# Performance work log

Hardware: AMD Instinct MI355X
Metric: run time of the kernel (lower is better)

Reference implementation:

```python
import jax, jax.numpy as jnp
import numpy as np

N_NODES, N_EDGES = 100000, 1600000
D_IN, D_HID, D_OUT = 128, 128, 64


def setup_inputs() -> dict:
    key = jax.random.key(0)
    k = jax.random.split(key, 6)
    x = jax.random.normal(k[0], (N_NODES, D_IN), dtype=jnp.float32)
    edge_index = jax.random.randint(k[1], (2, N_EDGES), 0, N_NODES, dtype=jnp.int32)
    # GCNConv params: W stored as [in, out] for right-multiply, glorot-ish scale
    W1 = jax.random.normal(k[2], (D_IN, D_HID), dtype=jnp.float32) * (1.0 / np.sqrt(D_IN))
    b1 = jnp.zeros((D_HID,), dtype=jnp.float32)
    W2 = jax.random.normal(k[3], (D_HID, D_OUT), dtype=jnp.float32) * (1.0 / np.sqrt(D_HID))
    b2 = jnp.zeros((D_OUT,), dtype=jnp.float32)
    return {"x": x, "edge_index": edge_index, "W1": W1, "b1": b1, "W2": W2, "b2": b2}


def reference(x, edge_index, W1, b1, W2, b2):
    N = x.shape[0]
    loops = jnp.arange(N, dtype=edge_index.dtype)
    src = jnp.concatenate([edge_index[0], loops])  # [E+N]
    dst = jnp.concatenate([edge_index[1], loops])  # [E+N]
    # symmetric GCN normalization (deg over targets, incl. self loops)
    deg = jax.ops.segment_sum(jnp.ones_like(dst, dtype=x.dtype), dst, num_segments=N)
    dinv = jnp.where(deg > 0, jax.lax.rsqrt(deg), 0.0)
    norm = dinv[src] * dinv[dst]  # [E+N]

    def gcn(h, W, b):
        h = h @ W                         # [N, out]
        msg = h[src] * norm[:, None]      # gather + scale, [E+N, out]
        return jax.ops.segment_sum(msg, dst, num_segments=N) + b

    h = jax.nn.relu(gcn(x, W1, b1))  # Dropout is identity in eval
    return gcn(h, W2, b2)
```

## Files before the change

### kernel.cpp

```cpp
#include <hip/hip_runtime.h>


#define D_IN  128
#define D_HID 128
#define D_OUT 64
#define NBSHIFT 9

typedef short short8 __attribute__((ext_vector_type(8)));
typedef float floatx4 __attribute__((ext_vector_type(4)));

__device__ __forceinline__ unsigned short f2bf(float f) {
    unsigned int u = __float_as_uint(f);
    u += 0x7fffu + ((u >> 16) & 1u);
    return (unsigned short)(u >> 16);
}
__device__ __forceinline__ float bf2f(unsigned short h) {
    return __uint_as_float((unsigned int)h << 16);
}
__device__ __forceinline__ float bf_lo(unsigned int u) { return __uint_as_float(u << 16); }
__device__ __forceinline__ float bf_hi(unsigned int u) { return __uint_as_float(u & 0xffff0000u); }


__global__ __launch_bounds__(256) void k_zero_int(int* __restrict__ p, int n) {
    int i = blockIdx.x * 256 + threadIdx.x;
    if (i < n) p[i] = 0;
}

__global__ __launch_bounds__(256) void k_bhist(const int* __restrict__ dst,
                                               int* __restrict__ bcnt, int E, int NB) {
    __shared__ int h[256];
    const int t = threadIdx.x;
    h[t] = 0;
    __syncthreads();
    const int base = blockIdx.x * 8192;
#pragma unroll
    for (int k = 0; k < 32; ++k) {
        int e = base + k * 256 + t;
        if (e < E) atomicAdd(&h[dst[e] >> NBSHIFT], 1);
    }
    __syncthreads();
    if (t < NB && h[t]) atomicAdd(&bcnt[t], h[t]);
}

__global__ __launch_bounds__(256) void k_bscan(const int* __restrict__ bcnt,
                                               int* __restrict__ bbase,
                                               int* __restrict__ bcur, int NB, int E) {
    __shared__ int ls[256];
    const int t = threadIdx.x;
    int v = (t < NB) ? bcnt[t] : 0;
    ls[t] = v;
    __syncthreads();
    for (int off = 1; off < 256; off <<= 1) {
        int y = (t >= off) ? ls[t - off] : 0;
        __syncthreads();
        ls[t] += y;
        __syncthreads();
    }
    if (t < NB) {
        bbase[t] = ls[t] - v;
        bcur[t]  = ls[t] - v;
    }
    if (t == 0) bbase[NB] = E;
}

__global__ __launch_bounds__(256) void k_bin(const int* __restrict__ src,
                                             const int* __restrict__ dst,
                                             int2* __restrict__ ebuf,
                                             int* __restrict__ bcur, int E, int NB) {
    __shared__ int h[256];
    __shared__ int basep[256];
    const int t = threadIdx.x;
    h[t] = 0;
    __syncthreads();
    const int base = blockIdx.x * 4096;
    int s[16], d[16];
#pragma unroll
    for (int k = 0; k < 16; ++k) {
        int e = base + k * 256 + t;
        bool v = e < E;
        s[k] = v ? src[e] : 0;
        d[k] = v ? dst[e] : -1;
        if (v) atomicAdd(&h[d[k] >> NBSHIFT], 1);
    }
    __syncthreads();
    if (t < NB && h[t]) basep[t] = atomicAdd(&bcur[t], h[t]);
    __syncthreads();
    h[t] = 0;
    __syncthreads();
#pragma unroll
    for (int k = 0; k < 16; ++k) {
        if (d[k] >= 0) {
            int b = d[k] >> NBSHIFT;
            int r = atomicAdd(&h[b], 1);
            ebuf[basep[b] + r] = make_int2(s[k], d[k]);
        }
    }
}

__global__ __launch_bounds__(256) void k_bfill(const int2* __restrict__ ebuf,
                                               const int* __restrict__ bbase,
                                               int* __restrict__ csr,
                                               int* __restrict__ rowstart,
                                               float* __restrict__ dinv,
                                               int N, int NB, int E) {
    __shared__ int cnt[512];
    __shared__ int pref[512];
    __shared__ int tsum[256];
    const int t = threadIdx.x;
    const int b = blockIdx.x;
    const int nb0 = b << NBSHIFT;
    const int NN = min(512, N - nb0);
    const int e0 = bbase[b], e1 = bbase[b + 1];

    cnt[t] = 0;
    cnt[t + 256] = 0;
    __syncthreads();
    for (int e = e0 + t; e < e1; e += 256)
        atomicAdd(&cnt[ebuf[e].y - nb0], 1);
    __syncthreads();

    int a0 = cnt[2 * t], a1 = cnt[2 * t + 1];
    tsum[t] = a0 + a1;
    __syncthreads();
    for (int off = 1; off < 256; off <<= 1) {
        int y = (t >= off) ? tsum[t - off] : 0;
        __syncthreads();
        tsum[t] += y;
        __syncthreads();
    }
    int excl = tsum[t] - (a0 + a1);
    pref[2 * t] = excl;
    pref[2 * t + 1] = excl + a0;
    __syncthreads();

    for (int nl = t; nl < NN; nl += 256) {
        rowstart[nb0 + nl] = e0 + pref[nl];
        dinv[nb0 + nl] = rsqrtf((float)(cnt[nl] + 1));
    }
    if (b == NB - 1 && t == 0) rowstart[N] = E;
    __syncthreads();

    for (int e = e0 + t; e < e1; e += 256) {
        int2 ed = ebuf[e];
        int r = atomicAdd(&pref[ed.y - nb0], 1);
        csr[e0 + r] = ed.x;
    }
}

__global__ void k_zero_pad(unsigned short* __restrict__ h1b,
                           unsigned short* __restrict__ h2b, int N) {
    int t = threadIdx.x;
    if (t < 128) h1b[(size_t)N * 128 + t] = 0;
    if (t < 64)  h2b[(size_t)N * 64 + t] = 0;
}


template <int DOUT_>
__global__ __launch_bounds__(256) void k_wsplit(const float* __restrict__ W,
                                                unsigned short* __restrict__ Ws) {
    constexpr int NCT = DOUT_ / 16;
    constexpr int HALF = 4 * NCT * 64 * 8;
    int id = blockIdx.x * 256 + threadIdx.x;
    if (id >= HALF) return;
    int i = id & 7;
    int lane = (id >> 3) & 63;
    int ctkt = id >> 9;
    int ct = ctkt % NCT, kt = ctkt / NCT;
    int k = kt * 32 + ((lane >> 4) << 3) + i;
    int n = ct * 16 + (lane & 15);
    float v = W[(size_t)k * DOUT_ + n];
    unsigned short h = f2bf(v);
    Ws[id] = h;
    Ws[HALF + id] = f2bf(v - bf2f(h));
}


template <int DOUT_>
__global__ __launch_bounds__(256) void mfma_gemm(const float* __restrict__ X,
                                                 const unsigned short* __restrict__ Wsplit,
                                                 const float* __restrict__ dinv,
                                                 unsigned short* __restrict__ Hb,
                                                 int N) {
    constexpr int NCT = DOUT_ / 16;
    constexpr int HALF = 4 * NCT * 64 * 8;
    __shared__ unsigned short lds[2 * HALF];

    const int t = threadIdx.x;
    {
        const int4* s4 = (const int4*)Wsplit;
        int4* d4 = (int4*)lds;
        constexpr int NV = 2 * HALF / 8;
        for (int i = t; i < NV; i += 256) d4[i] = s4[i];
    }
    __syncthreads();

    const int wave = t >> 6, lane = t & 63;
    const int grow = blockIdx.x * 64 + wave * 16 + (lane & 15);
    const int rowc = min(grow, N - 1);
    const int kl = (lane >> 4) << 3;

    floatx4 acc[NCT];
#pragma unroll
    for (int c = 0; c < NCT; ++c) acc[c] = (floatx4)0.f;

#pragma unroll
    for (int kt = 0; kt < 4; ++kt) {
        const float* xp = X + (size_t)rowc * 128 + kt * 32 + kl;
        float4 a0 = *(const float4*)xp;
        float4 a1 = *(const float4*)(xp + 4);
        float xs[8] = {a0.x, a0.y, a0.z, a0.w, a1.x, a1.y, a1.z, a1.w};
        short8 ah, al;
#pragma unroll
        for (int i = 0; i < 8; ++i) {
            unsigned short h = f2bf(xs[i]);
            ah[i] = (short)h;
            al[i] = (short)f2bf(xs[i] - bf2f(h));
        }
#pragma unroll
        for (int c = 0; c < NCT; ++c) {
            const int off = ((kt * NCT + c) * 64 + lane) * 8;
            short8 bh = *(const short8*)&lds[off];
            short8 bl = *(const short8*)&lds[HALF + off];
            acc[c] = __builtin_amdgcn_mfma_f32_16x16x32_bf16(ah, bh, acc[c], 0, 0, 0);
            acc[c] = __builtin_amdgcn_mfma_f32_16x16x32_bf16(al, bh, acc[c], 0, 0, 0);
            acc[c] = __builtin_amdgcn_mfma_f32_16x16x32_bf16(ah, bl, acc[c], 0, 0, 0);
        }
    }

    const int orow = blockIdx.x * 64 + wave * 16 + ((lane >> 4) << 2);
#pragma unroll
    for (int r = 0; r < 4; ++r) {
        int gr = orow + r;
        if (gr < N) {
            float dn = dinv[gr];
#pragma unroll
            for (int c = 0; c < NCT; ++c)
                Hb[(size_t)gr * DOUT_ + c * 16 + (lane & 15)] = f2bf(acc[c][r] * dn);
        }
    }
}


template <int DOUT_>
__global__ __launch_bounds__(256) void mfma_gemm_b(const unsigned short* __restrict__ Xb,
                                                   const unsigned short* __restrict__ Wsplit,
                                                   const float* __restrict__ dinv,
                                                   unsigned short* __restrict__ Hb,
                                                   int N) {
    constexpr int NCT = DOUT_ / 16;
    constexpr int HALF = 4 * NCT * 64 * 8;
    __shared__ unsigned short lds[2 * HALF];

    const int t = threadIdx.x;
    {
        const int4* s4 = (const int4*)Wsplit;
        int4* d4 = (int4*)lds;
        constexpr int NV = 2 * HALF / 8;
        for (int i = t; i < NV; i += 256) d4[i] = s4[i];
    }
    __syncthreads();

    const int wave = t >> 6, lane = t & 63;
    const int grow = blockIdx.x * 64 + wave * 16 + (lane & 15);
    const int rowc = min(grow, N - 1);
    const int kl = (lane >> 4) << 3;

    floatx4 acc[NCT];
#pragma unroll
    for (int c = 0; c < NCT; ++c) acc[c] = (floatx4)0.f;

#pragma unroll
    for (int kt = 0; kt < 4; ++kt) {
        short8 ah = *(const short8*)(Xb + (size_t)rowc * 128 + kt * 32 + kl);
#pragma unroll
        for (int c = 0; c < NCT; ++c) {
            const int off = ((kt * NCT + c) * 64 + lane) * 8;
            short8 bh = *(const short8*)&lds[off];
            short8 bl = *(const short8*)&lds[HALF + off];
            acc[c] = __builtin_amdgcn_mfma_f32_16x16x32_bf16(ah, bh, acc[c], 0, 0, 0);
            acc[c] = __builtin_amdgcn_mfma_f32_16x16x32_bf16(ah, bl, acc[c], 0, 0, 0);
        }
    }

    const int orow = blockIdx.x * 64 + wave * 16 + ((lane >> 4) << 2);
#pragma unroll
    for (int r = 0; r < 4; ++r) {
        int gr = orow + r;
        if (gr < N) {
            float dn = dinv[gr];
#pragma unroll
            for (int c = 0; c < NCT; ++c)
                Hb[(size_t)gr * DOUT_ + c * 16 + (lane & 15)] = f2bf(acc[c][r] * dn);
        }
    }
}


__global__ __launch_bounds__(256) void agg1_kernel(const uint4* __restrict__ H4,
                                                   const int* __restrict__ rowstart,
                                                   const int* __restrict__ csr_src,
                                                   const float* __restrict__ dinv,
                                                   const float* __restrict__ bias,
                                                   unsigned short* __restrict__ outb,
                                                   int N, int NBK) {
    const int xcd = blockIdx.x & 7;
    const int ch  = xcd >> 2;
    const int nb  = (blockIdx.x >> 3) * 4 + (xcd & 3);
    if (nb >= NBK) return;
    const int t = threadIdx.x;
    const int wave = t >> 6, lane = t & 63;
    const int g = lane >> 3, gl = lane & 7;
    const int n = nb * 32 + wave * 8 + g;
    const bool live = n < N;
    const int e0 = live ? rowstart[n] : 0;
    const int deg = live ? rowstart[n + 1] - e0 : 0;
    int m = deg;
    m = max(m, __shfl_xor(m, 8));
    m = max(m, __shfl_xor(m, 16));
    m = max(m, __shfl_xor(m, 32));

    const int cb = ch * 8;
    float acc[8] = {0.f, 0.f, 0.f, 0.f, 0.f, 0.f, 0.f, 0.f};
    for (int eb = 0; eb < m; eb += 8) {
        int s_l = (eb + gl < deg) ? csr_src[e0 + eb + gl] : N;
        int sj[8]; uint4 u[8];
#pragma unroll
        for (int q = 0; q < 8; ++q) sj[q] = __shfl(s_l, (g << 3) | q);
#pragma unroll
        for (int q = 0; q < 8; ++q) u[q] = H4[(size_t)sj[q] * 16 + cb + gl];
#pragma unroll
        for (int q = 0; q < 8; ++q) {
            acc[0] += bf_lo(u[q].x); acc[1] += bf_hi(u[q].x);
            acc[2] += bf_lo(u[q].y); acc[3] += bf_hi(u[q].y);
            acc[4] += bf_lo(u[q].z); acc[5] += bf_hi(u[q].z);
            acc[6] += bf_lo(u[q].w); acc[7] += bf_hi(u[q].w);
        }
    }
    uint4 us = H4[(size_t)(live ? n : N) * 16 + cb + gl];
    acc[0] += bf_lo(us.x); acc[1] += bf_hi(us.x);
    acc[2] += bf_lo(us.y); acc[3] += bf_hi(us.y);
    acc[4] += bf_lo(us.z); acc[5] += bf_hi(us.z);
    acc[6] += bf_lo(us.w); acc[7] += bf_hi(us.w);

    if (live) {
        const float dn = dinv[n];
        const float* bp = bias + ch * 64 + gl * 8;
        unsigned short o[8];
#pragma unroll
        for (int j = 0; j < 8; ++j)
            o[j] = f2bf(fmaxf(fmaf(acc[j], dn, bp[j]), 0.f));
        *reinterpret_cast<int4*>(&outb[(size_t)n * 128 + ch * 64 + gl * 8]) =
            *reinterpret_cast<const int4*>(o);
    }
}

__global__ __launch_bounds__(256) void agg2_kernel(const uint4* __restrict__ H4,
                                                   const int* __restrict__ rowstart,
                                                   const int* __restrict__ csr_src,
                                                   const float* __restrict__ dinv,
                                                   const float* __restrict__ bias,
                                                   float* __restrict__ out, int N) {
    const int t = threadIdx.x;
    const int wave = t >> 6, lane = t & 63;
    const int g = lane >> 3, gl = lane & 7;
    const int n = blockIdx.x * 32 + wave * 8 + g;
    const bool live = n < N;
    const int e0 = live ? rowstart[n] : 0;
    const int e1 = live ? rowstart[n + 1] : 0;
    const int deg = e1 - e0;
    int m = deg;
    m = max(m, __shfl_xor(m, 8));
    m = max(m, __shfl_xor(m, 16));
    m = max(m, __shfl_xor(m, 32));

    float acc[8] = {0.f, 0.f, 0.f, 0.f, 0.f, 0.f, 0.f, 0.f};
    for (int eb = 0; eb < m; eb += 8) {
        int s_l = (eb + gl < deg) ? csr_src[e0 + eb + gl] : N;
        int sj[8]; uint4 u[8];
#pragma unroll
        for (int q = 0; q < 8; ++q) sj[q] = __shfl(s_l, (g << 3) | q);
#pragma unroll
        for (int q = 0; q < 8; ++q) u[q] = H4[(size_t)sj[q] * 8 + gl];
#pragma unroll
        for (int q = 0; q < 8; ++q) {
            acc[0] += bf_lo(u[q].x); acc[1] += bf_hi(u[q].x);
            acc[2] += bf_lo(u[q].y); acc[3] += bf_hi(u[q].y);
            acc[4] += bf_lo(u[q].z); acc[5] += bf_hi(u[q].z);
            acc[6] += bf_lo(u[q].w); acc[7] += bf_hi(u[q].w);
        }
    }
    uint4 us = H4[(size_t)(live ? n : N) * 8 + gl];
    acc[0] += bf_lo(us.x); acc[1] += bf_hi(us.x);
    acc[2] += bf_lo(us.y); acc[3] += bf_hi(us.y);
    acc[4] += bf_lo(us.z); acc[5] += bf_hi(us.z);
    acc[6] += bf_lo(us.w); acc[7] += bf_hi(us.w);

    if (live) {
        const float dn = dinv[n];
        float4 o0, o1;
        o0.x = fmaf(acc[0], dn, bias[gl * 8 + 0]);
        o0.y = fmaf(acc[1], dn, bias[gl * 8 + 1]);
        o0.z = fmaf(acc[2], dn, bias[gl * 8 + 2]);
        o0.w = fmaf(acc[3], dn, bias[gl * 8 + 3]);
        o1.x = fmaf(acc[4], dn, bias[gl * 8 + 4]);
        o1.y = fmaf(acc[5], dn, bias[gl * 8 + 5]);
        o1.z = fmaf(acc[6], dn, bias[gl * 8 + 6]);
        o1.w = fmaf(acc[7], dn, bias[gl * 8 + 7]);
        float* op = out + (size_t)n * 64 + gl * 8;
        *reinterpret_cast<float4*>(op) = o0;
        *reinterpret_cast<float4*>(op + 4) = o1;
    }
}


extern "C" void kernel_launch(void* const* d_in, const int* in_sizes, int n_in,
                              void* d_out, int out_size, void* d_ws, size_t ws_size,
                              hipStream_t stream) {
    const float* x  = (const float*)d_in[0];
    const int*   ei = (const int*)d_in[1];
    const float* W1 = (const float*)d_in[2];
    const float* b1 = (const float*)d_in[3];
    const float* W2 = (const float*)d_in[4];
    const float* b2 = (const float*)d_in[5];
    float* out = (float*)d_out;

    const int N = in_sizes[0] / D_IN;
    const int E = in_sizes[1] / 2;
    const int* src = ei;
    const int* dst = ei + E;
    const int NB = (N + 511) >> NBSHIFT;

    char* w = (char*)d_ws;
    auto alloc = [&](size_t bytes) {
        char* p = w;
        w += (bytes + 255) & ~(size_t)255;
        return p;
    };
    int*   rowstart  = (int*)alloc((size_t)(N + 1) * 4);
    float* dinv      = (float*)alloc((size_t)N * 4);
    int*   csr       = (int*)alloc((size_t)E * 4);
    unsigned short* h1b = (unsigned short*)alloc((size_t)(N + 1) * D_HID * 2);
    unsigned short* h2b = (unsigned short*)alloc((size_t)(N + 1) * D_OUT * 2);
    unsigned short* hgb = (unsigned short*)alloc((size_t)N * D_HID * 2);
    int*   bcnt      = (int*)alloc((size_t)NB * 4);
    int*   bbase     = (int*)alloc((size_t)(NB + 1) * 4);
    int*   bcur      = (int*)alloc((size_t)NB * 4);
    unsigned short* w1s = (unsigned short*)alloc(2 * 4 * (D_HID / 16) * 64 * 8 * 2);
    unsigned short* w2s = (unsigned short*)alloc(2 * 4 * (D_OUT / 16) * 64 * 8 * 2);
    int2*  ebuf      = (int2*)hgb;

    k_zero_int<<<1, 256, 0, stream>>>(bcnt, NB);
    k_bhist<<<(E + 8191) / 8192, 256, 0, stream>>>(dst, bcnt, E, NB);
    k_bscan<<<1, 256, 0, stream>>>(bcnt, bbase, bcur, NB, E);
    k_bin<<<(E + 4095) / 4096, 256, 0, stream>>>(src, dst, ebuf, bcur, E, NB);
    k_bfill<<<NB, 256, 0, stream>>>(ebuf, bbase, csr, rowstart, dinv, N, NB, E);
    k_zero_pad<<<1, 128, 0, stream>>>(h1b, h2b, N);
    k_wsplit<D_HID><<<(4 * (D_HID / 16) * 64 * 8 + 255) / 256, 256, 0, stream>>>(W1, w1s);
    k_wsplit<D_OUT><<<(4 * (D_OUT / 16) * 64 * 8 + 255) / 256, 256, 0, stream>>>(W2, w2s);

    mfma_gemm<D_HID><<<(N + 63) / 64, 256, 0, stream>>>(x, w1s, dinv, h1b, N);

    const int NBK = (N + 31) / 32;
    agg1_kernel<<<((NBK + 3) / 4) * 8, 256, 0, stream>>>((const uint4*)h1b, rowstart, csr,
                                                         dinv, b1, hgb, N, NBK);
    mfma_gemm_b<D_OUT><<<(N + 63) / 64, 256, 0, stream>>>(hgb, w2s, dinv, h2b, N);
    agg2_kernel<<<(N + 31) / 32, 256, 0, stream>>>((const uint4*)h2b, rowstart, csr,
                                                   dinv, b2, out, N);
}
```

Measured before the change: 198.0 us.

## Store hidden features column-chunked and partition aggregation by 16-wide feature slices

```diff
diff --git a/kernel.cpp b/kernel.cpp
--- a/kernel.cpp
+++ b/kernel.cpp
@@ -150,8 +150,8 @@
 __global__ void k_zero_pad(unsigned short* __restrict__ h1b,
                            unsigned short* __restrict__ h2b, int N) {
     int t = threadIdx.x;
-    if (t < 128) h1b[(size_t)N * 128 + t] = 0;
-    if (t < 64)  h2b[(size_t)N * 64 + t] = 0;
+    if (t < 128) h1b[((size_t)(t >> 4) * (N + 1) + N) * 16 + (t & 15)] = 0;
+    if (t < 64)  h2b[((size_t)(t >> 4) * (N + 1) + N) * 16 + (t & 15)] = 0;
 }
 
 
@@ -235,7 +235,7 @@
             float dn = dinv[gr];
 #pragma unroll
             for (int c = 0; c < NCT; ++c)
-                Hb[(size_t)gr * DOUT_ + c * 16 + (lane & 15)] = f2bf(acc[c][r] * dn);
+                Hb[((size_t)c * (N + 1) + gr) * 16 + (lane & 15)] = f2bf(acc[c][r] * dn);
         }
     }
 }
@@ -271,7 +271,8 @@
 
 #pragma unroll
     for (int kt = 0; kt < 4; ++kt) {
-        short8 ah = *(const short8*)(Xb + (size_t)rowc * 128 + kt * 32 + kl);
+        const int k0 = kt * 32 + kl;
+        short8 ah = *(const short8*)&Xb[((size_t)(k0 >> 4) * N + rowc) * 16 + (k0 & 15)];
 #pragma unroll
         for (int c = 0; c < NCT; ++c) {
             const int off = ((kt * NCT + c) * 64 + lane) * 8;
@@ -290,7 +291,7 @@
             float dn = dinv[gr];
 #pragma unroll
             for (int c = 0; c < NCT; ++c)
-                Hb[(size_t)gr * DOUT_ + c * 16 + (lane & 15)] = f2bf(acc[c][r] * dn);
+                Hb[((size_t)c * (N + 1) + gr) * 16 + (lane & 15)] = f2bf(acc[c][r] * dn);
         }
     }
 }
@@ -301,33 +302,36 @@
                                                    const int* __restrict__ csr_src,
                                                    const float* __restrict__ dinv,
                                                    const float* __restrict__ bias,
-                                                   unsigned short* __restrict__ outb,
-                                                   int N, int NBK) {
-    const int xcd = blockIdx.x & 7;
-    const int ch  = xcd >> 2;
-    const int nb  = (blockIdx.x >> 3) * 4 + (xcd & 3);
-    if (nb >= NBK) return;
+                                                   unsigned short* __restrict__ outc,
+                                                   int N) {
+    const int p = blockIdx.x & 7;
+    const int chunk = blockIdx.x >> 3;
     const int t = threadIdx.x;
     const int wave = t >> 6, lane = t & 63;
-    const int g = lane >> 3, gl = lane & 7;
-    const int n = nb * 32 + wave * 8 + g;
-    const bool live = n < N;
-    const int e0 = live ? rowstart[n] : 0;
-    const int deg = live ? rowstart[n + 1] - e0 : 0;
-    int m = deg;
-    m = max(m, __shfl_xor(m, 8));
-    m = max(m, __shfl_xor(m, 16));
-    m = max(m, __shfl_xor(m, 32));
-
-    const int cb = ch * 8;
+    const int g = lane >> 1, gl = lane & 1;
+    const int n = chunk * 128 + wave * 32 + g;
+    if (n >= N) return;
+    const uint4* __restrict__ Hp = H4 + (size_t)p * (N + 1) * 2;
+    const int e0 = rowstart[n];
+    const int deg = rowstart[n + 1] - e0;
+
     float acc[8] = {0.f, 0.f, 0.f, 0.f, 0.f, 0.f, 0.f, 0.f};
-    for (int eb = 0; eb < m; eb += 8) {
-        int s_l = (eb + gl < deg) ? csr_src[e0 + eb + gl] : N;
-        int sj[8]; uint4 u[8];
-#pragma unroll
-        for (int q = 0; q < 8; ++q) sj[q] = __shfl(s_l, (g << 3) | q);
-#pragma unroll
-        for (int q = 0; q < 8; ++q) u[q] = H4[(size_t)sj[q] * 16 + cb + gl];
+    for (int eb = 0; eb < deg; eb += 8) {
+        int s[4];
+#pragma unroll
+        for (int k = 0; k < 4; ++k) {
+            int idx = eb + 2 * k + gl;
+            s[k] = (idx < deg) ? __builtin_nontemporal_load(csr_src + e0 + idx) : N;
+        }
+        int sj[8];
+#pragma unroll
+        for (int k = 0; k < 4; ++k) {
+            sj[2 * k]     = __shfl(s[k], (g << 1));
+            sj[2 * k + 1] = __shfl(s[k], (g << 1) | 1);
+        }
+        uint4 u[8];
+#pragma unroll
+        for (int q = 0; q < 8; ++q) u[q] = Hp[(size_t)sj[q] * 2 + gl];
 #pragma unroll
         for (int q = 0; q < 8; ++q) {
             acc[0] += bf_lo(u[q].x); acc[1] += bf_hi(u[q].x);
@@ -336,22 +340,20 @@
             acc[6] += bf_lo(u[q].w); acc[7] += bf_hi(u[q].w);
         }
     }
-    uint4 us = H4[(size_t)(live ? n : N) * 16 + cb + gl];
+    uint4 us = Hp[(size_t)n * 2 + gl];
     acc[0] += bf_lo(us.x); acc[1] += bf_hi(us.x);
     acc[2] += bf_lo(us.y); acc[3] += bf_hi(us.y);
     acc[4] += bf_lo(us.z); acc[5] += bf_hi(us.z);
     acc[6] += bf_lo(us.w); acc[7] += bf_hi(us.w);
 
-    if (live) {
-        const float dn = dinv[n];
-        const float* bp = bias + ch * 64 + gl * 8;
-        unsigned short o[8];
-#pragma unroll
-        for (int j = 0; j < 8; ++j)
-            o[j] = f2bf(fmaxf(fmaf(acc[j], dn, bp[j]), 0.f));
-        *reinterpret_cast<int4*>(&outb[(size_t)n * 128 + ch * 64 + gl * 8]) =
-            *reinterpret_cast<const int4*>(o);
-    }
+    const float dn = dinv[n];
+    const float* bp = bias + p * 16 + gl * 8;
+    unsigned short o[8];
+#pragma unroll
+    for (int j = 0; j < 8; ++j)
+        o[j] = f2bf(fmaxf(fmaf(acc[j], dn, bp[j]), 0.f));
+    *reinterpret_cast<uint4*>(&outc[((size_t)p * N + n) * 16 + gl * 8]) =
+        *reinterpret_cast<const uint4*>(o);
 }
 
 __global__ __launch_bounds__(256) void agg2_kernel(const uint4* __restrict__ H4,
@@ -359,28 +361,38 @@
                                                    const int* __restrict__ csr_src,
                                                    const float* __restrict__ dinv,
                                                    const float* __restrict__ bias,
-                                                   float* __restrict__ out, int N) {
+                                                   float* __restrict__ out,
+                                                   int N, int NCH) {
+    const int slot = blockIdx.x & 7;
+    const int p = slot & 3;
+    const int chunk = (blockIdx.x >> 3) * 2 + (slot >> 2);
+    if (chunk >= NCH) return;
     const int t = threadIdx.x;
     const int wave = t >> 6, lane = t & 63;
-    const int g = lane >> 3, gl = lane & 7;
-    const int n = blockIdx.x * 32 + wave * 8 + g;
-    const bool live = n < N;
-    const int e0 = live ? rowstart[n] : 0;
-    const int e1 = live ? rowstart[n + 1] : 0;
-    const int deg = e1 - e0;
-    int m = deg;
-    m = max(m, __shfl_xor(m, 8));
-    m = max(m, __shfl_xor(m, 16));
-    m = max(m, __shfl_xor(m, 32));
+    const int g = lane >> 1, gl = lane & 1;
+    const int n = chunk * 128 + wave * 32 + g;
+    if (n >= N) return;
+    const uint4* __restrict__ Hp = H4 + (size_t)p * (N + 1) * 2;
+    const int e0 = rowstart[n];
+    const int deg = rowstart[n + 1] - e0;
 
     float acc[8] = {0.f, 0.f, 0.f, 0.f, 0.f, 0.f, 0.f, 0.f};
-    for (int eb = 0; eb < m; eb += 8) {
-        int s_l = (eb + gl < deg) ? csr_src[e0 + eb + gl] : N;
-        int sj[8]; uint4 u[8];
-#pragma unroll
-        for (int q = 0; q < 8; ++q) sj[q] = __shfl(s_l, (g << 3) | q);
-#pragma unroll
-        for (int q = 0; q < 8; ++q) u[q] = H4[(size_t)sj[q] * 8 + gl];
+    for (int eb = 0; eb < deg; eb += 8) {
+        int s[4];
+#pragma unroll
+        for (int k = 0; k < 4; ++k) {
+            int idx = eb + 2 * k + gl;
+            s[k] = (idx < deg) ? __builtin_nontemporal_load(csr_src + e0 + idx) : N;
+        }
+        int sj[8];
+#pragma unroll
+        for (int k = 0; k < 4; ++k) {
+            sj[2 * k]     = __shfl(s[k], (g << 1));
+            sj[2 * k + 1] = __shfl(s[k], (g << 1) | 1);
+        }
+        uint4 u[8];
+#pragma unroll
+        for (int q = 0; q < 8; ++q) u[q] = Hp[(size_t)sj[q] * 2 + gl];
 #pragma unroll
         for (int q = 0; q < 8; ++q) {
             acc[0] += bf_lo(u[q].x); acc[1] += bf_hi(u[q].x);
@@ -389,27 +401,26 @@
             acc[6] += bf_lo(u[q].w); acc[7] += bf_hi(u[q].w);
         }
     }
-    uint4 us = H4[(size_t)(live ? n : N) * 8 + gl];
+    uint4 us = Hp[(size_t)n * 2 + gl];
     acc[0] += bf_lo(us.x); acc[1] += bf_hi(us.x);
     acc[2] += bf_lo(us.y); acc[3] += bf_hi(us.y);
     acc[4] += bf_lo(us.z); acc[5] += bf_hi(us.z);
     acc[6] += bf_lo(us.w); acc[7] += bf_hi(us.w);
 
-    if (live) {
-        const float dn = dinv[n];
-        float4 o0, o1;
-        o0.x = fmaf(acc[0], dn, bias[gl * 8 + 0]);
-        o0.y = fmaf(acc[1], dn, bias[gl * 8 + 1]);
-        o0.z = fmaf(acc[2], dn, bias[gl * 8 + 2]);
-        o0.w = fmaf(acc[3], dn, bias[gl * 8 + 3]);
-        o1.x = fmaf(acc[4], dn, bias[gl * 8 + 4]);
-        o1.y = fmaf(acc[5], dn, bias[gl * 8 + 5]);
-        o1.z = fmaf(acc[6], dn, bias[gl * 8 + 6]);
-        o1.w = fmaf(acc[7], dn, bias[gl * 8 + 7]);
-        float* op = out + (size_t)n * 64 + gl * 8;
-        *reinterpret_cast<float4*>(op) = o0;
-        *reinterpret_cast<float4*>(op + 4) = o1;
-    }
+    const float dn = dinv[n];
+    const float* bp = bias + p * 16 + gl * 8;
+    float4 o0, o1;
+    o0.x = fmaf(acc[0], dn, bp[0]);
+    o0.y = fmaf(acc[1], dn, bp[1]);
+    o0.z = fmaf(acc[2], dn, bp[2]);
+    o0.w = fmaf(acc[3], dn, bp[3]);
+    o1.x = fmaf(acc[4], dn, bp[4]);
+    o1.y = fmaf(acc[5], dn, bp[5]);
+    o1.z = fmaf(acc[6], dn, bp[6]);
+    o1.w = fmaf(acc[7], dn, bp[7]);
+    float* op = out + (size_t)n * 64 + p * 16 + gl * 8;
+    *reinterpret_cast<float4*>(op) = o0;
+    *reinterpret_cast<float4*>(op + 4) = o1;
 }
 
 
@@ -458,12 +469,12 @@
     k_wsplit<D_HID><<<(4 * (D_HID / 16) * 64 * 8 + 255) / 256, 256, 0, stream>>>(W1, w1s);
     k_wsplit<D_OUT><<<(4 * (D_OUT / 16) * 64 * 8 + 255) / 256, 256, 0, stream>>>(W2, w2s);
 
+    const int NCH = (N + 127) / 128;
+
     mfma_gemm<D_HID><<<(N + 63) / 64, 256, 0, stream>>>(x, w1s, dinv, h1b, N);
-
-    const int NBK = (N + 31) / 32;
-    agg1_kernel<<<((NBK + 3) / 4) * 8, 256, 0, stream>>>((const uint4*)h1b, rowstart, csr,
-                                                         dinv, b1, hgb, N, NBK);
+    agg1_kernel<<<NCH * 8, 256, 0, stream>>>((const uint4*)h1b, rowstart, csr,
+                                             dinv, b1, hgb, N);
     mfma_gemm_b<D_OUT><<<(N + 63) / 64, 256, 0, stream>>>(hgb, w2s, dinv, h2b, N);
-    agg2_kernel<<<(N + 31) / 32, 256, 0, stream>>>((const uint4*)h2b, rowstart, csr,
-                                                   dinv, b2, out, N);
-}
+    agg2_kernel<<<((NCH + 1) / 2) * 8, 256, 0, stream>>>((const uint4*)h2b, rowstart, csr,
+                                                         dinv, b2, out, N, NCH);
+}
```

Measured after the change: 308.2 us. 1.56x slower.

## Pack binned edges into one int and sort CSR neighbors by source octant

Applied to the files above, without the earlier changes.

```diff
diff --git a/kernel.cpp b/kernel.cpp
--- a/kernel.cpp
+++ b/kernel.cpp
@@ -8,6 +8,7 @@
 
 typedef short short8 __attribute__((ext_vector_type(8)));
 typedef float floatx4 __attribute__((ext_vector_type(4)));
+typedef float floatx2 __attribute__((ext_vector_type(2)));
 
 __device__ __forceinline__ unsigned short f2bf(float f) {
     unsigned int u = __float_as_uint(f);
@@ -65,7 +66,7 @@
 
 __global__ __launch_bounds__(256) void k_bin(const int* __restrict__ src,
                                              const int* __restrict__ dst,
-                                             int2* __restrict__ ebuf,
+                                             int* __restrict__ ebuf,
                                              int* __restrict__ bcur, int E, int NB) {
     __shared__ int h[256];
     __shared__ int basep[256];
@@ -92,19 +93,19 @@
         if (d[k] >= 0) {
             int b = d[k] >> NBSHIFT;
             int r = atomicAdd(&h[b], 1);
-            ebuf[basep[b] + r] = make_int2(s[k], d[k]);
-        }
-    }
-}
-
-__global__ __launch_bounds__(256) void k_bfill(const int2* __restrict__ ebuf,
+            ebuf[basep[b] + r] = (s[k] << 9) | (d[k] & 511);
+        }
+    }
+}
+
+__global__ __launch_bounds__(256) void k_bfill(const int* __restrict__ ebuf,
                                                const int* __restrict__ bbase,
                                                int* __restrict__ csr,
                                                int* __restrict__ rowstart,
                                                float* __restrict__ dinv,
-                                               int N, int NB, int E) {
-    __shared__ int cnt[512];
-    __shared__ int pref[512];
+                                               int N, int NB, int E, int qshift) {
+    __shared__ int cnt2[512][8];
+    __shared__ int nbase[512];
     __shared__ int tsum[256];
     const int t = threadIdx.x;
     const int b = blockIdx.x;
@@ -112,15 +113,23 @@
     const int NN = min(512, N - nb0);
     const int e0 = bbase[b], e1 = bbase[b + 1];
 
-    cnt[t] = 0;
-    cnt[t + 256] = 0;
-    __syncthreads();
-    for (int e = e0 + t; e < e1; e += 256)
-        atomicAdd(&cnt[ebuf[e].y - nb0], 1);
-    __syncthreads();
-
-    int a0 = cnt[2 * t], a1 = cnt[2 * t + 1];
-    tsum[t] = a0 + a1;
+    for (int i = t; i < 512 * 8; i += 256) ((int*)cnt2)[i] = 0;
+    __syncthreads();
+    for (int e = e0 + t; e < e1; e += 256) {
+        int v = ebuf[e];
+        int nl = v & 511;
+        int o = ((unsigned)v >> 9) >> qshift;
+        atomicAdd(&cnt2[nl][o], 1);
+    }
+    __syncthreads();
+
+    int deg0 = 0, deg1 = 0;
+#pragma unroll
+    for (int o = 0; o < 8; ++o) {
+        deg0 += cnt2[2 * t][o];
+        deg1 += cnt2[2 * t + 1][o];
+    }
+    tsum[t] = deg0 + deg1;
     __syncthreads();
     for (int off = 1; off < 256; off <<= 1) {
         int y = (t >= off) ? tsum[t - off] : 0;
@@ -128,22 +137,37 @@
         tsum[t] += y;
         __syncthreads();
     }
-    int excl = tsum[t] - (a0 + a1);
-    pref[2 * t] = excl;
-    pref[2 * t + 1] = excl + a0;
-    __syncthreads();
-
+    int excl = tsum[t] - (deg0 + deg1);
+    nbase[2 * t] = excl;
+    nbase[2 * t + 1] = excl + deg0;
+    __syncthreads();
+
+#pragma unroll
+    for (int k = 0; k < 2; ++k) {
+        int nl = 2 * t + k;
+        int run = nbase[nl];
+#pragma unroll
+        for (int o = 0; o < 8; ++o) {
+            int c = cnt2[nl][o];
+            cnt2[nl][o] = run;
+            run += c;
+        }
+    }
     for (int nl = t; nl < NN; nl += 256) {
-        rowstart[nb0 + nl] = e0 + pref[nl];
-        dinv[nb0 + nl] = rsqrtf((float)(cnt[nl] + 1));
+        int deg = ((nl < 511 ? nbase[nl + 1] : e1 - e0)) - nbase[nl];
+        rowstart[nb0 + nl] = e0 + nbase[nl];
+        dinv[nb0 + nl] = rsqrtf((float)(deg + 1));
     }
     if (b == NB - 1 && t == 0) rowstart[N] = E;
     __syncthreads();
 
     for (int e = e0 + t; e < e1; e += 256) {
-        int2 ed = ebuf[e];
-        int r = atomicAdd(&pref[ed.y - nb0], 1);
-        csr[e0 + r] = ed.x;
+        int v = ebuf[e];
+        int nl = v & 511;
+        int srcv = (unsigned)v >> 9;
+        int o = srcv >> qshift;
+        int r = atomicAdd(&cnt2[nl][o], 1);
+        csr[e0 + r] = srcv;
     }
 }
 
@@ -322,7 +346,9 @@
     const int cb = ch * 8;
     float acc[8] = {0.f, 0.f, 0.f, 0.f, 0.f, 0.f, 0.f, 0.f};
     for (int eb = 0; eb < m; eb += 8) {
-        int s_l = (eb + gl < deg) ? csr_src[e0 + eb + gl] : N;
+        int s_l = (eb + gl < deg)
+                      ? __builtin_nontemporal_load(csr_src + e0 + eb + gl)
+                      : N;
         int sj[8]; uint4 u[8];
 #pragma unroll
         for (int q = 0; q < 8; ++q) sj[q] = __shfl(s_l, (g << 3) | q);
@@ -366,8 +392,7 @@
     const int n = blockIdx.x * 32 + wave * 8 + g;
     const bool live = n < N;
     const int e0 = live ? rowstart[n] : 0;
-    const int e1 = live ? rowstart[n + 1] : 0;
-    const int deg = e1 - e0;
+    const int deg = live ? rowstart[n + 1] - e0 : 0;
     int m = deg;
     m = max(m, __shfl_xor(m, 8));
     m = max(m, __shfl_xor(m, 16));
@@ -375,7 +400,9 @@
 
     float acc[8] = {0.f, 0.f, 0.f, 0.f, 0.f, 0.f, 0.f, 0.f};
     for (int eb = 0; eb < m; eb += 8) {
-        int s_l = (eb + gl < deg) ? csr_src[e0 + eb + gl] : N;
+        int s_l = (eb + gl < deg)
+                      ? __builtin_nontemporal_load(csr_src + e0 + eb + gl)
+                      : N;
         int sj[8]; uint4 u[8];
 #pragma unroll
         for (int q = 0; q < 8; ++q) sj[q] = __shfl(s_l, (g << 3) | q);
@@ -397,18 +424,19 @@
 
     if (live) {
         const float dn = dinv[n];
-        float4 o0, o1;
-        o0.x = fmaf(acc[0], dn, bias[gl * 8 + 0]);
-        o0.y = fmaf(acc[1], dn, bias[gl * 8 + 1]);
-        o0.z = fmaf(acc[2], dn, bias[gl * 8 + 2]);
-        o0.w = fmaf(acc[3], dn, bias[gl * 8 + 3]);
-        o1.x = fmaf(acc[4], dn, bias[gl * 8 + 4]);
-        o1.y = fmaf(acc[5], dn, bias[gl * 8 + 5]);
-        o1.z = fmaf(acc[6], dn, bias[gl * 8 + 6]);
-        o1.w = fmaf(acc[7], dn, bias[gl * 8 + 7]);
+        const float* bp = bias + gl * 8;
+        floatx4 o0, o1;
+        o0.x = fmaf(acc[0], dn, bp[0]);
+        o0.y = fmaf(acc[1], dn, bp[1]);
+        o0.z = fmaf(acc[2], dn, bp[2]);
+        o0.w = fmaf(acc[3], dn, bp[3]);
+        o1.x = fmaf(acc[4], dn, bp[4]);
+        o1.y = fmaf(acc[5], dn, bp[5]);
+        o1.z = fmaf(acc[6], dn, bp[6]);
+        o1.w = fmaf(acc[7], dn, bp[7]);
         float* op = out + (size_t)n * 64 + gl * 8;
-        *reinterpret_cast<float4*>(op) = o0;
-        *reinterpret_cast<float4*>(op + 4) = o1;
+        __builtin_nontemporal_store(o0, reinterpret_cast<floatx4*>(op));
+        __builtin_nontemporal_store(o1, reinterpret_cast<floatx4*>(op + 4));
     }
 }
 
@@ -429,6 +457,8 @@
     const int* src = ei;
     const int* dst = ei + E;
     const int NB = (N + 511) >> NBSHIFT;
+    int qshift = 0;
+    while (((N - 1) >> qshift) >= 8) ++qshift;
 
     char* w = (char*)d_ws;
     auto alloc = [&](size_t bytes) {
@@ -447,13 +477,13 @@
     int*   bcur      = (int*)alloc((size_t)NB * 4);
     unsigned short* w1s = (unsigned short*)alloc(2 * 4 * (D_HID / 16) * 64 * 8 * 2);
     unsigned short* w2s = (unsigned short*)alloc(2 * 4 * (D_OUT / 16) * 64 * 8 * 2);
-    int2*  ebuf      = (int2*)hgb;
+    int*   ebuf      = (int*)hgb;
 
     k_zero_int<<<1, 256, 0, stream>>>(bcnt, NB);
     k_bhist<<<(E + 8191) / 8192, 256, 0, stream>>>(dst, bcnt, E, NB);
     k_bscan<<<1, 256, 0, stream>>>(bcnt, bbase, bcur, NB, E);
     k_bin<<<(E + 4095) / 4096, 256, 0, stream>>>(src, dst, ebuf, bcur, E, NB);
-    k_bfill<<<NB, 256, 0, stream>>>(ebuf, bbase, csr, rowstart, dinv, N, NB, E);
+    k_bfill<<<NB, 256, 0, stream>>>(ebuf, bbase, csr, rowstart, dinv, N, NB, E, qshift);
     k_zero_pad<<<1, 128, 0, stream>>>(h1b, h2b, N);
     k_wsplit<D_HID><<<(4 * (D_HID / 16) * 64 * 8 + 255) / 256, 256, 0, stream>>>(W1, w1s);
     k_wsplit<D_OUT><<<(4 * (D_OUT / 16) * 64 * 8 + 255) / 256, 256, 0, stream>>>(W2, w2s);
```

Result: slower. 204.5 us (+3.3%).

## Replace global bucket histogram/scan with fixed-size segments and packed edge/node info

Applied to the files above, without the earlier changes.

```diff
diff --git a/kernel.cpp b/kernel.cpp
--- a/kernel.cpp
+++ b/kernel.cpp
@@ -5,6 +5,7 @@
 #define D_HID 128
 #define D_OUT 64
 #define NBSHIFT 9
+#define SEG 10240
 
 typedef short short8 __attribute__((ext_vector_type(8)));
 typedef float floatx4 __attribute__((ext_vector_type(4)));
@@ -21,150 +22,13 @@
 __device__ __forceinline__ float bf_hi(unsigned int u) { return __uint_as_float(u & 0xffff0000u); }
 
 
-__global__ __launch_bounds__(256) void k_zero_int(int* __restrict__ p, int n) {
-    int i = blockIdx.x * 256 + threadIdx.x;
-    if (i < n) p[i] = 0;
-}
-
-__global__ __launch_bounds__(256) void k_bhist(const int* __restrict__ dst,
-                                               int* __restrict__ bcnt, int E, int NB) {
-    __shared__ int h[256];
-    const int t = threadIdx.x;
-    h[t] = 0;
-    __syncthreads();
-    const int base = blockIdx.x * 8192;
-#pragma unroll
-    for (int k = 0; k < 32; ++k) {
-        int e = base + k * 256 + t;
-        if (e < E) atomicAdd(&h[dst[e] >> NBSHIFT], 1);
-    }
-    __syncthreads();
-    if (t < NB && h[t]) atomicAdd(&bcnt[t], h[t]);
-}
-
-__global__ __launch_bounds__(256) void k_bscan(const int* __restrict__ bcnt,
-                                               int* __restrict__ bbase,
-                                               int* __restrict__ bcur, int NB, int E) {
-    __shared__ int ls[256];
-    const int t = threadIdx.x;
-    int v = (t < NB) ? bcnt[t] : 0;
-    ls[t] = v;
-    __syncthreads();
-    for (int off = 1; off < 256; off <<= 1) {
-        int y = (t >= off) ? ls[t - off] : 0;
-        __syncthreads();
-        ls[t] += y;
-        __syncthreads();
-    }
-    if (t < NB) {
-        bbase[t] = ls[t] - v;
-        bcur[t]  = ls[t] - v;
-    }
-    if (t == 0) bbase[NB] = E;
-}
-
-__global__ __launch_bounds__(256) void k_bin(const int* __restrict__ src,
-                                             const int* __restrict__ dst,
-                                             int2* __restrict__ ebuf,
-                                             int* __restrict__ bcur, int E, int NB) {
-    __shared__ int h[256];
-    __shared__ int basep[256];
-    const int t = threadIdx.x;
-    h[t] = 0;
-    __syncthreads();
-    const int base = blockIdx.x * 4096;
-    int s[16], d[16];
-#pragma unroll
-    for (int k = 0; k < 16; ++k) {
-        int e = base + k * 256 + t;
-        bool v = e < E;
-        s[k] = v ? src[e] : 0;
-        d[k] = v ? dst[e] : -1;
-        if (v) atomicAdd(&h[d[k] >> NBSHIFT], 1);
-    }
-    __syncthreads();
-    if (t < NB && h[t]) basep[t] = atomicAdd(&bcur[t], h[t]);
-    __syncthreads();
-    h[t] = 0;
-    __syncthreads();
-#pragma unroll
-    for (int k = 0; k < 16; ++k) {
-        if (d[k] >= 0) {
-            int b = d[k] >> NBSHIFT;
-            int r = atomicAdd(&h[b], 1);
-            ebuf[basep[b] + r] = make_int2(s[k], d[k]);
-        }
-    }
-}
-
-__global__ __launch_bounds__(256) void k_bfill(const int2* __restrict__ ebuf,
-                                               const int* __restrict__ bbase,
-                                               int* __restrict__ csr,
-                                               int* __restrict__ rowstart,
-                                               float* __restrict__ dinv,
-                                               int N, int NB, int E) {
-    __shared__ int cnt[512];
-    __shared__ int pref[512];
-    __shared__ int tsum[256];
-    const int t = threadIdx.x;
-    const int b = blockIdx.x;
-    const int nb0 = b << NBSHIFT;
-    const int NN = min(512, N - nb0);
-    const int e0 = bbase[b], e1 = bbase[b + 1];
-
-    cnt[t] = 0;
-    cnt[t + 256] = 0;
-    __syncthreads();
-    for (int e = e0 + t; e < e1; e += 256)
-        atomicAdd(&cnt[ebuf[e].y - nb0], 1);
-    __syncthreads();
-
-    int a0 = cnt[2 * t], a1 = cnt[2 * t + 1];
-    tsum[t] = a0 + a1;
-    __syncthreads();
-    for (int off = 1; off < 256; off <<= 1) {
-        int y = (t >= off) ? tsum[t - off] : 0;
-        __syncthreads();
-        tsum[t] += y;
-        __syncthreads();
-    }
-    int excl = tsum[t] - (a0 + a1);
-    pref[2 * t] = excl;
-    pref[2 * t + 1] = excl + a0;
-    __syncthreads();
-
-    for (int nl = t; nl < NN; nl += 256) {
-        rowstart[nb0 + nl] = e0 + pref[nl];
-        dinv[nb0 + nl] = rsqrtf((float)(cnt[nl] + 1));
-    }
-    if (b == NB - 1 && t == 0) rowstart[N] = E;
-    __syncthreads();
-
-    for (int e = e0 + t; e < e1; e += 256) {
-        int2 ed = ebuf[e];
-        int r = atomicAdd(&pref[ed.y - nb0], 1);
-        csr[e0 + r] = ed.x;
-    }
-}
-
-__global__ void k_zero_pad(unsigned short* __restrict__ h1b,
-                           unsigned short* __restrict__ h2b, int N) {
-    int t = threadIdx.x;
-    if (t < 128) h1b[(size_t)N * 128 + t] = 0;
-    if (t < 64)  h2b[(size_t)N * 64 + t] = 0;
-}
-
-
-template <int DOUT_>
-__global__ __launch_bounds__(256) void k_wsplit(const float* __restrict__ W,
-                                                unsigned short* __restrict__ Ws) {
-    constexpr int NCT = DOUT_ / 16;
-    constexpr int HALF = 4 * NCT * 64 * 8;
-    int id = blockIdx.x * 256 + threadIdx.x;
-    if (id >= HALF) return;
+__device__ __forceinline__ void wsplit_one(const float* __restrict__ W,
+                                           unsigned short* __restrict__ Ws,
+                                           int id, int DOUT_, int HALF) {
     int i = id & 7;
     int lane = (id >> 3) & 63;
     int ctkt = id >> 9;
+    int NCT = DOUT_ / 16;
     int ct = ctkt % NCT, kt = ctkt / NCT;
     int k = kt * 32 + ((lane >> 4) << 3) + i;
     int n = ct * 16 + (lane & 15);
@@ -172,6 +36,107 @@
     unsigned short h = f2bf(v);
     Ws[id] = h;
     Ws[HALF + id] = f2bf(v - bf2f(h));
+}
+
+__global__ __launch_bounds__(256) void k_prep(const float* __restrict__ W1,
+                                              const float* __restrict__ W2,
+                                              unsigned short* __restrict__ w1s,
+                                              unsigned short* __restrict__ w2s,
+                                              unsigned short* __restrict__ h1b,
+                                              unsigned short* __restrict__ h2b,
+                                              int* __restrict__ bcur, int N) {
+    int id = blockIdx.x * 256 + threadIdx.x;
+    if (id < 16384) wsplit_one(W1, w1s, id, D_HID, 16384);
+    if (id < 8192)  wsplit_one(W2, w2s, id, D_OUT, 8192);
+    if (id < 128)   h1b[(size_t)N * 128 + id] = 0;
+    if (id < 64)    h2b[(size_t)N * 64 + id] = 0;
+    if (id < 256)   bcur[id] = 0;
+}
+
+
+__global__ __launch_bounds__(256) void k_bin(const int* __restrict__ src,
+                                             const int* __restrict__ dst,
+                                             int* __restrict__ ebuf,
+                                             int* __restrict__ bcur, int E, int NB) {
+    __shared__ int h[256];
+    __shared__ int basep[256];
+    const int t = threadIdx.x;
+    h[t] = 0;
+    __syncthreads();
+    const int base = blockIdx.x * 4096;
+    int s[16], d[16];
+#pragma unroll
+    for (int k = 0; k < 16; ++k) {
+        int e = base + k * 256 + t;
+        bool v = e < E;
+        s[k] = v ? src[e] : 0;
+        d[k] = v ? dst[e] : -1;
+        if (v) atomicAdd(&h[d[k] >> NBSHIFT], 1);
+    }
+    __syncthreads();
+    if (t < NB && h[t]) basep[t] = atomicAdd(&bcur[t], h[t]);
+    __syncthreads();
+    h[t] = 0;
+    __syncthreads();
+#pragma unroll
+    for (int k = 0; k < 16; ++k) {
+        if (d[k] >= 0) {
+            int b = d[k] >> NBSHIFT;
+            int r = atomicAdd(&h[b], 1);
+            ebuf[(size_t)b * SEG + basep[b] + r] = (s[k] << 9) | (d[k] & 511);
+        }
+    }
+}
+
+__global__ __launch_bounds__(256) void k_bfill(const int* __restrict__ ebuf,
+                                               const int* __restrict__ bcur,
+                                               int* __restrict__ csr,
+                                               int* __restrict__ nodeinfo,
+                                               float* __restrict__ dinv,
+                                               int N) {
+    __shared__ int cnt[512];
+    __shared__ int pref[512];
+    __shared__ int tsum[256];
+    const int t = threadIdx.x;
+    const int b = blockIdx.x;
+    const int nb0 = b << NBSHIFT;
+    const int NN = min(512, N - nb0);
+    const int ec = bcur[b];
+    const int* __restrict__ eb = ebuf + (size_t)b * SEG;
+
+    cnt[t] = 0;
+    cnt[t + 256] = 0;
+    __syncthreads();
+    for (int e = t; e < ec; e += 256) atomicAdd(&cnt[eb[e] & 511], 1);
+    __syncthreads();
+
+    int a0 = cnt[2 * t], a1 = cnt[2 * t + 1];
+    tsum[t] = a0 + a1;
+    __syncthreads();
+    for (int off = 1; off < 256; off <<= 1) {
+        int y = (t >= off) ? tsum[t - off] : 0;
+        __syncthreads();
+        tsum[t] += y;
+        __syncthreads();
+    }
+    int excl = tsum[t] - (a0 + a1);
+    pref[2 * t] = excl;
+    pref[2 * t + 1] = excl + a0;
+    __syncthreads();
+
+    const int segbase = b * SEG;
+    for (int nl = t; nl < NN; nl += 256) {
+        int deg = cnt[nl];
+        nodeinfo[nb0 + nl] = ((segbase + pref[nl]) << 10) | deg;
+        dinv[nb0 + nl] = rsqrtf((float)(deg + 1));
+    }
+    __syncthreads();
+
+    for (int e = t; e < ec; e += 256) {
+        int v = eb[e];
+        int r = atomicAdd(&pref[v & 511], 1);
+        csr[segbase + r] = (unsigned)v >> 9;
+    }
 }
 
 
@@ -297,7 +262,7 @@
 
 
 __global__ __launch_bounds__(256) void agg1_kernel(const uint4* __restrict__ H4,
-                                                   const int* __restrict__ rowstart,
+                                                   const int* __restrict__ nodeinfo,
                                                    const int* __restrict__ csr_src,
                                                    const float* __restrict__ dinv,
                                                    const float* __restrict__ bias,
@@ -312,8 +277,9 @@
     const int g = lane >> 3, gl = lane & 7;
     const int n = nb * 32 + wave * 8 + g;
     const bool live = n < N;
-    const int e0 = live ? rowstart[n] : 0;
-    const int deg = live ? rowstart[n + 1] - e0 : 0;
+    const int v = live ? nodeinfo[n] : 0;
+    const int e0 = (unsigned)v >> 10;
+    const int deg = v & 1023;
     int m = deg;
     m = max(m, __shfl_xor(m, 8));
     m = max(m, __shfl_xor(m, 16));
@@ -322,7 +288,9 @@
     const int cb = ch * 8;
     float acc[8] = {0.f, 0.f, 0.f, 0.f, 0.f, 0.f, 0.f, 0.f};
     for (int eb = 0; eb < m; eb += 8) {
-        int s_l = (eb + gl < deg) ? csr_src[e0 + eb + gl] : N;
+        int s_l = (eb + gl < deg)
+                      ? __builtin_nontemporal_load(csr_src + e0 + eb + gl)
+                      : N;
         int sj[8]; uint4 u[8];
 #pragma unroll
         for (int q = 0; q < 8; ++q) sj[q] = __shfl(s_l, (g << 3) | q);
@@ -354,61 +322,61 @@
     }
 }
 
-__global__ __launch_bounds__(256) void agg2_kernel(const uint4* __restrict__ H4,
-                                                   const int* __restrict__ rowstart,
+__global__ __launch_bounds__(256) void agg2_kernel(const uint2* __restrict__ H2,
+                                                   const int* __restrict__ nodeinfo,
                                                    const int* __restrict__ csr_src,
                                                    const float* __restrict__ dinv,
                                                    const float* __restrict__ bias,
-                                                   float* __restrict__ out, int N) {
+                                                   float* __restrict__ out,
+                                                   int N, int NBK) {
+    const int xcd = blockIdx.x & 7;
+    const int ch  = xcd >> 2;
+    const int nb  = (blockIdx.x >> 3) * 4 + (xcd & 3);
+    if (nb >= NBK) return;
     const int t = threadIdx.x;
     const int wave = t >> 6, lane = t & 63;
     const int g = lane >> 3, gl = lane & 7;
-    const int n = blockIdx.x * 32 + wave * 8 + g;
+    const int n = nb * 32 + wave * 8 + g;
     const bool live = n < N;
-    const int e0 = live ? rowstart[n] : 0;
-    const int e1 = live ? rowstart[n + 1] : 0;
-    const int deg = e1 - e0;
+    const int v = live ? nodeinfo[n] : 0;
+    const int e0 = (unsigned)v >> 10;
+    const int deg = v & 1023;
     int m = deg;
     m = max(m, __shfl_xor(m, 8));
     m = max(m, __shfl_xor(m, 16));
     m = max(m, __shfl_xor(m, 32));
 
-    float acc[8] = {0.f, 0.f, 0.f, 0.f, 0.f, 0.f, 0.f, 0.f};
+    const int cb = ch * 8;
+    float acc[4] = {0.f, 0.f, 0.f, 0.f};
     for (int eb = 0; eb < m; eb += 8) {
-        int s_l = (eb + gl < deg) ? csr_src[e0 + eb + gl] : N;
-        int sj[8]; uint4 u[8];
+        int s_l = (eb + gl < deg)
+                      ? __builtin_nontemporal_load(csr_src + e0 + eb + gl)
+                      : N;
+        int sj[8]; uint2 u[8];
 #pragma unroll
         for (int q = 0; q < 8; ++q) sj[q] = __shfl(s_l, (g << 3) | q);
 #pragma unroll
-        for (int q = 0; q < 8; ++q) u[q] = H4[(size_t)sj[q] * 8 + gl];
+        for (int q = 0; q < 8; ++q) u[q] = H2[(size_t)sj[q] * 16 + cb + gl];
 #pragma unroll
         for (int q = 0; q < 8; ++q) {
             acc[0] += bf_lo(u[q].x); acc[1] += bf_hi(u[q].x);
             acc[2] += bf_lo(u[q].y); acc[3] += bf_hi(u[q].y);
-            acc[4] += bf_lo(u[q].z); acc[5] += bf_hi(u[q].z);
-            acc[6] += bf_lo(u[q].w); acc[7] += bf_hi(u[q].w);
-        }
-    }
-    uint4 us = H4[(size_t)(live ? n : N) * 8 + gl];
+        }
+    }
+    uint2 us = H2[(size_t)(live ? n : N) * 16 + cb + gl];
     acc[0] += bf_lo(us.x); acc[1] += bf_hi(us.x);
     acc[2] += bf_lo(us.y); acc[3] += bf_hi(us.y);
-    acc[4] += bf_lo(us.z); acc[5] += bf_hi(us.z);
-    acc[6] += bf_lo(us.w); acc[7] += bf_hi(us.w);
 
     if (live) {
         const float dn = dinv[n];
-        float4 o0, o1;
-        o0.x = fmaf(acc[0], dn, bias[gl * 8 + 0]);
-        o0.y = fmaf(acc[1], dn, bias[gl * 8 + 1]);
-        o0.z = fmaf(acc[2], dn, bias[gl * 8 + 2]);
-        o0.w = fmaf(acc[3], dn, bias[gl * 8 + 3]);
-        o1.x = fmaf(acc[4], dn, bias[gl * 8 + 4]);
-        o1.y = fmaf(acc[5], dn, bias[gl * 8 + 5]);
-        o1.z = fmaf(acc[6], dn, bias[gl * 8 + 6]);
-        o1.w = fmaf(acc[7], dn, bias[gl * 8 + 7]);
-        float* op = out + (size_t)n * 64 + gl * 8;
-        *reinterpret_cast<float4*>(op) = o0;
-        *reinterpret_cast<float4*>(op + 4) = o1;
+        const int c0 = ch * 32 + gl * 4;
+        const float* bp = bias + c0;
+        floatx4 o;
+        o.x = fmaf(acc[0], dn, bp[0]);
+        o.y = fmaf(acc[1], dn, bp[1]);
+        o.z = fmaf(acc[2], dn, bp[2]);
+        o.w = fmaf(acc[3], dn, bp[3]);
+        __builtin_nontemporal_store(o, reinterpret_cast<floatx4*>(&out[(size_t)n * 64 + c0]));
     }
 }
 
@@ -436,34 +404,27 @@
         w += (bytes + 255) & ~(size_t)255;
         return p;
     };
-    int*   rowstart  = (int*)alloc((size_t)(N + 1) * 4);
+    int*   nodeinfo  = (int*)alloc((size_t)N * 4);
     float* dinv      = (float*)alloc((size_t)N * 4);
-    int*   csr       = (int*)alloc((size_t)E * 4);
+    int*   csr       = (int*)alloc((size_t)NB * SEG * 4);
     unsigned short* h1b = (unsigned short*)alloc((size_t)(N + 1) * D_HID * 2);
     unsigned short* h2b = (unsigned short*)alloc((size_t)(N + 1) * D_OUT * 2);
     unsigned short* hgb = (unsigned short*)alloc((size_t)N * D_HID * 2);
-    int*   bcnt      = (int*)alloc((size_t)NB * 4);
-    int*   bbase     = (int*)alloc((size_t)(NB + 1) * 4);
-    int*   bcur      = (int*)alloc((size_t)NB * 4);
-    unsigned short* w1s = (unsigned short*)alloc(2 * 4 * (D_HID / 16) * 64 * 8 * 2);
-    unsigned short* w2s = (unsigned short*)alloc(2 * 4 * (D_OUT / 16) * 64 * 8 * 2);
-    int2*  ebuf      = (int2*)hgb;
-
-    k_zero_int<<<1, 256, 0, stream>>>(bcnt, NB);
-    k_bhist<<<(E + 8191) / 8192, 256, 0, stream>>>(dst, bcnt, E, NB);
-    k_bscan<<<1, 256, 0, stream>>>(bcnt, bbase, bcur, NB, E);
+    int*   bcur      = (int*)alloc(256 * 4);
+    unsigned short* w1s = (unsigned short*)alloc(2 * 16384 * 2);
+    unsigned short* w2s = (unsigned short*)alloc(2 * 8192 * 2);
+    int*   ebuf      = (int*)hgb;
+
+    k_prep<<<64, 256, 0, stream>>>(W1, W2, w1s, w2s, h1b, h2b, bcur, N);
     k_bin<<<(E + 4095) / 4096, 256, 0, stream>>>(src, dst, ebuf, bcur, E, NB);
-    k_bfill<<<NB, 256, 0, stream>>>(ebuf, bbase, csr, rowstart, dinv, N, NB, E);
-    k_zero_pad<<<1, 128, 0, stream>>>(h1b, h2b, N);
-    k_wsplit<D_HID><<<(4 * (D_HID / 16) * 64 * 8 + 255) / 256, 256, 0, stream>>>(W1, w1s);
-    k_wsplit<D_OUT><<<(4 * (D_OUT / 16) * 64 * 8 + 255) / 256, 256, 0, stream>>>(W2, w2s);
+    k_bfill<<<NB, 256, 0, stream>>>(ebuf, bcur, csr, nodeinfo, dinv, N);
 
     mfma_gemm<D_HID><<<(N + 63) / 64, 256, 0, stream>>>(x, w1s, dinv, h1b, N);
 
     const int NBK = (N + 31) / 32;
-    agg1_kernel<<<((NBK + 3) / 4) * 8, 256, 0, stream>>>((const uint4*)h1b, rowstart, csr,
+    agg1_kernel<<<((NBK + 3) / 4) * 8, 256, 0, stream>>>((const uint4*)h1b, nodeinfo, csr,
                                                          dinv, b1, hgb, N, NBK);
     mfma_gemm_b<D_OUT><<<(N + 63) / 64, 256, 0, stream>>>(hgb, w2s, dinv, h2b, N);
-    agg2_kernel<<<(N + 31) / 32, 256, 0, stream>>>((const uint4*)h2b, rowstart, csr,
-                                                   dinv, b2, out, N);
-}
+    agg2_kernel<<<((NBK + 3) / 4) * 8, 256, 0, stream>>>((const uint2*)h2b, nodeinfo, csr,
+                                                         dinv, b2, out, N, NBK);
+}
```

Result: slower. 205.1 us (+3.6%).
